# Optimization experiments

Measured on AMD Instinct MI355X. Metric: run time of the kernel, lower is better.

The kernel has to match this reference:

```python
import jax, jax.numpy as jnp
import numpy as np

EMBED_DIM = 768
NUM_HEADS = 12
HEAD_DIM = EMBED_DIM // NUM_HEADS
SCALE = HEAD_DIM ** -0.5


def setup_inputs() -> dict:
    key = jax.random.key(0)
    k_x, k_wqkv, k_bqkv, k_wfc, k_bfc = jax.random.split(key, 5)
    B, S, D = 32, 577, EMBED_DIM
    x = jax.random.normal(k_x, (B, S, D), dtype=jnp.float32)
    # torch Linear default init ~ U(-1/sqrt(fan_in), 1/sqrt(fan_in)); scale suffices
    lim = 1.0 / np.sqrt(D)
    w_qkv = jax.random.uniform(k_wqkv, (D, 3 * D), jnp.float32, -lim, lim)
    b_qkv = jax.random.uniform(k_bqkv, (3 * D,), jnp.float32, -lim, lim)
    w_fc = jax.random.uniform(k_wfc, (D, D), jnp.float32, -lim, lim)
    b_fc = jax.random.uniform(k_bfc, (D,), jnp.float32, -lim, lim)
    return {"x": x, "w_qkv": w_qkv, "b_qkv": b_qkv, "w_fc": w_fc, "b_fc": b_fc}


def reference(x, w_qkv, b_qkv, w_fc, b_fc):
    B, S, D = x.shape
    H, Dh = NUM_HEADS, HEAD_DIM
    qkv = x @ w_qkv + b_qkv                      # [B,S,3D]
    qkv = qkv.reshape(B, S, 3, H, Dh)
    q, k, v = jnp.moveaxis(qkv, 2, 0)            # each [B,S,H,Dh]
    # scores: [B,H,S,S]
    attn = jnp.einsum('bqhd,bkhd->bhqk', q, k) * SCALE
    attn = jax.nn.softmax(attn, axis=-1)
    out = jnp.einsum('bhqk,bkhd->bqhd', attn, v).reshape(B, S, D)
    # dropout in eval mode -> identity
    return out @ w_fc + b_fc
```

## Files before the change

### kernel.cpp

```cpp
#include <hip/hip_runtime.h>
#include <hip/hip_bf16.h>
#include <stdint.h>

typedef __attribute__((ext_vector_type(8))) short short8;
typedef __attribute__((ext_vector_type(4))) float f32x4;

typedef __attribute__((address_space(3))) uint8_t lds_u8;
typedef __attribute__((address_space(1))) uint8_t glb_u8;

__device__ __forceinline__ void load_lds_16(const void* g, void* l) {
    __builtin_amdgcn_global_load_lds((glb_u8*)g, (lds_u8*)l, 16, 0, 0);
}

__device__ __forceinline__ unsigned short f2b(float f) {
    __hip_bfloat16 h = __float2bfloat16(f);
    return __builtin_bit_cast(unsigned short, h);
}
__device__ __forceinline__ ushort2 f2b2(float a, float b) {
    __hip_bfloat162 h = __float22bfloat162_rn(float2{a, b});
    ushort2 r;
    __builtin_memcpy(&r, &h, sizeof(r));
    return r;
}
__device__ __forceinline__ float b2f(unsigned short u) {
    unsigned int x = ((unsigned int)u) << 16;
    return __builtin_bit_cast(float, x);
}

constexpr int Bz = 32, Ss = 577, Dd = 768, Hh = 12;
constexpr int Mm = Bz * Ss;
constexpr int QKV_N = 3 * Dd;
constexpr float SCALE_L2E = 0.125f * 1.4426950408889634f;

__global__ void cast_f32_bf16(const float* __restrict__ src,
                              unsigned short* __restrict__ dst, int n4) {
    int i = blockIdx.x * blockDim.x + threadIdx.x;
    if (i >= n4) return;
    float4 v = ((const float4*)src)[i];
    ushort4 o;
    o.x = f2b(v.x); o.y = f2b(v.y); o.z = f2b(v.z); o.w = f2b(v.w);
    ((ushort4*)dst)[i] = o;
}

__global__ void transpose_cast(const float* __restrict__ src,
                               unsigned short* __restrict__ dst, int R, int C) {
    __shared__ unsigned short tile[32][33];
    int c0 = blockIdx.x * 32, r0 = blockIdx.y * 32;
    int tx = threadIdx.x, ty = threadIdx.y;
#pragma unroll
    for (int i = 0; i < 4; ++i)
        tile[ty + i * 8][tx] = f2b(src[(size_t)(r0 + ty + i * 8) * C + c0 + tx]);
    __syncthreads();
#pragma unroll
    for (int i = 0; i < 4; ++i) {
        int rr = ty + i * 8;
        dst[(size_t)(c0 + rr) * R + r0 + tx] = tile[tx][rr];
    }
}

template <int N_, bool OUT_BF16>
__global__ __launch_bounds__(512, 2)
void gemm256(const unsigned short* __restrict__ A,
             const unsigned short* __restrict__ Bt,
             const float* __restrict__ bias,
             void* __restrict__ Cout) {
    constexpr int K = 768;
    constexpr int KB = 12;
    constexpr int NX = N_ / 256;
    constexpr int NY = (Mm + 255) / 256;
    constexpr int NWG = NX * NY;
    constexpr int QC = NWG >> 3, RC = NWG & 7;
    extern __shared__ __align__(16) uint8_t smem[];

    const int tid = threadIdx.x;
    const int wave = tid >> 6, lane = tid & 63;
    const int quad = lane >> 4, lc = lane & 15;
    const int wm = wave >> 2, wn = wave & 3;

    const int orig = blockIdx.y * NX + blockIdx.x;
    const int xcd = orig & 7, lid = orig >> 3;
    const int wgid = (xcd < RC ? xcd * (QC + 1) : RC * (QC + 1) + (xcd - RC) * QC) + lid;
    const int tm = (wgid / NX) * 256;
    const int tn = (wgid % NX) * 256;

    const int colsw = ((lane & 7) ^ (lane >> 3)) * 8;
    const unsigned short* rpA[2][2];
    const unsigned short* rpB[2][2];
#pragma unroll
    for (int s = 0; s < 2; ++s) {
        const int prs = (s * 8 + wave) * 8 + (lane >> 3);
#pragma unroll
        for (int h = 0; h < 2; ++h) {
            int ar = tm + (prs >> 6) * 128 + h * 64 + (prs & 63);
            if (ar >= Mm) ar = Mm - 1;
            rpA[s][h] = A + (size_t)ar * K + colsw;
            int br = tn + (prs >> 5) * 64 + h * 32 + (prs & 31);
            rpB[s][h] = Bt + (size_t)br * K + colsw;
        }
    }

    auto ldsA = [&](int b, int mh) -> uint8_t* { return smem + b * 65536 + mh * 16384; };
    auto ldsB = [&](int b, int nh) -> uint8_t* { return smem + b * 65536 + 32768 + nh * 16384; };

    auto stageA = [&](int kb, int mh) {
        uint8_t* d = ldsA(kb & 1, mh) + wave * 1024;
        load_lds_16(rpA[0][mh] + kb * 64, d);
        load_lds_16(rpA[1][mh] + kb * 64, d + 8192);
    };
    auto stageB = [&](int kb, int nh) {
        uint8_t* d = ldsB(kb & 1, nh) + wave * 1024;
        load_lds_16(rpB[0][nh] + kb * 64, d);
        load_lds_16(rpB[1][nh] + kb * 64, d + 8192);
    };

    short8 af[2][4], bf[2][2];
    auto readA = [&](int b, int mh) {
        const unsigned short* p = (const unsigned short*)ldsA(b, mh);
#pragma unroll
        for (int i = 0; i < 4; ++i) {
            const int pr = wm * 64 + i * 16 + lc;
            const unsigned short* r = p + pr * 64;
            const int sw = pr & 7;
            af[0][i] = *(const short8*)(r + ((quad) ^ sw) * 8);
            af[1][i] = *(const short8*)(r + ((4 + quad) ^ sw) * 8);
        }
    };
    auto readB = [&](int b, int nh) {
        const unsigned short* p = (const unsigned short*)ldsB(b, nh);
#pragma unroll
        for (int j = 0; j < 2; ++j) {
            const int pr = wn * 32 + j * 16 + lc;
            const unsigned short* r = p + pr * 64;
            const int sw = pr & 7;
            bf[0][j] = *(const short8*)(r + ((quad) ^ sw) * 8);
            bf[1][j] = *(const short8*)(r + ((4 + quad) ^ sw) * 8);
        }
    };

    f32x4 acc[8][4] = {};
    auto quadmfma = [&](int mh, int nh) {
        __builtin_amdgcn_s_setprio(1);
#pragma unroll
        for (int ks = 0; ks < 2; ++ks)
#pragma unroll
            for (int i = 0; i < 4; ++i)
#pragma unroll
                for (int j = 0; j < 2; ++j)
                    acc[mh * 4 + i][nh * 2 + j] = __builtin_amdgcn_mfma_f32_16x16x32_bf16(
                        af[ks][i], bf[ks][j], acc[mh * 4 + i][nh * 2 + j], 0, 0, 0);
        __builtin_amdgcn_s_setprio(0);
    };

    stageA(0, 0); stageB(0, 1); stageA(0, 1); stageB(0, 0);
    stageA(1, 0); stageB(1, 1);
    asm volatile("s_waitcnt vmcnt(4)" ::: "memory");
    __builtin_amdgcn_s_barrier();

    for (int T = 0; T < KB; ++T) {
        const int rb = T & 1;
        readA(rb, 0); readB(rb, 0);
        if (T + 1 < KB) stageA(T + 1, 1);
        __builtin_amdgcn_s_barrier();
        asm volatile("s_waitcnt lgkmcnt(0)" ::: "memory");
        quadmfma(0, 0);
        __builtin_amdgcn_s_barrier();
        readB(rb, 1);
        if (T + 1 < KB) stageB(T + 1, 0);
        __builtin_amdgcn_s_barrier();
        asm volatile("s_waitcnt lgkmcnt(0)" ::: "memory");
        quadmfma(0, 1);
        __builtin_amdgcn_s_barrier();
        readA(rb, 1);
        if (T + 2 < KB) stageA(T + 2, 0);
        __builtin_amdgcn_s_barrier();
        asm volatile("s_waitcnt lgkmcnt(0)" ::: "memory");
        quadmfma(1, 1);
        __builtin_amdgcn_s_barrier();
        readB(rb, 0);
        if (T + 2 < KB) stageB(T + 2, 1);
        __builtin_amdgcn_s_barrier();
        asm volatile("s_waitcnt lgkmcnt(0)" ::: "memory");
        quadmfma(1, 0);
        if (T + 2 < KB) { asm volatile("s_waitcnt vmcnt(4)" ::: "memory"); }
        else            { asm volatile("s_waitcnt vmcnt(0)" ::: "memory"); }
        __builtin_amdgcn_s_barrier();
    }

    float bv[4];
#pragma unroll
    for (int j = 0; j < 4; ++j) bv[j] = bias[tn + wn * 64 + j * 16 + lc];

    float* ep = (float*)smem + wave * (16 * 68);
    const int erow = lane >> 2, ec = (lane & 3) * 16;
#pragma unroll
    for (int ia = 0; ia < 8; ++ia) {
#pragma unroll
        for (int j = 0; j < 4; ++j)
#pragma unroll
            for (int r = 0; r < 4; ++r)
                ep[(quad * 4 + r) * 68 + j * 16 + lc] = acc[ia][j][r] + bv[j];
        __threadfence_block();
        int grow = tm + wm * 128 + ia * 16 + erow;
        if (grow < Mm) {
            float4 c0 = *(float4*)&ep[erow * 68 + ec + 0];
            float4 c1 = *(float4*)&ep[erow * 68 + ec + 4];
            float4 c2 = *(float4*)&ep[erow * 68 + ec + 8];
            float4 c3 = *(float4*)&ep[erow * 68 + ec + 12];
            int gcol = tn + wn * 64 + ec;
            if constexpr (OUT_BF16) {
                unsigned short o[16];
                *(ushort2*)&o[0]  = f2b2(c0.x, c0.y);
                *(ushort2*)&o[2]  = f2b2(c0.z, c0.w);
                *(ushort2*)&o[4]  = f2b2(c1.x, c1.y);
                *(ushort2*)&o[6]  = f2b2(c1.z, c1.w);
                *(ushort2*)&o[8]  = f2b2(c2.x, c2.y);
                *(ushort2*)&o[10] = f2b2(c2.z, c2.w);
                *(ushort2*)&o[12] = f2b2(c3.x, c3.y);
                *(ushort2*)&o[14] = f2b2(c3.z, c3.w);
                unsigned short* op = (unsigned short*)Cout + (size_t)grow * N_ + gcol;
                *(short8*)(op + 0) = *(short8*)&o[0];
                *(short8*)(op + 8) = *(short8*)&o[8];
            } else {
                float* op = (float*)Cout + (size_t)grow * N_ + gcol;
                *(float4*)(op + 0)  = c0;
                *(float4*)(op + 4)  = c1;
                *(float4*)(op + 8)  = c2;
                *(float4*)(op + 12) = c3;
            }
        }
        __threadfence_block();
    }
}

__device__ __forceinline__ void attn_tile(
    const unsigned short* __restrict__ Ktile,
    const unsigned short* __restrict__ Vtb,
    unsigned short* __restrict__ Pqw,
    const short8& qf0, const short8& qf1,
    int quad, int lc,
    f32x4 (&oacc)[4], f32x4& lacc) {

    const int sw = lc & 7;
    f32x4 sfr[4];
    __builtin_amdgcn_s_setprio(1);
#pragma unroll
    for (int f = 0; f < 4; ++f) {
        const unsigned short* kr = Ktile + (f * 16 + lc) * 64;
        short8 k0 = *(const short8*)(kr + (quad ^ sw) * 8);
        short8 k1 = *(const short8*)(kr + ((quad ^ 4) ^ sw) * 8);
        f32x4 z = {};
        z = __builtin_amdgcn_mfma_f32_16x16x32_bf16(k0, qf0, z, 0, 0, 0);
        z = __builtin_amdgcn_mfma_f32_16x16x32_bf16(k1, qf1, z, 0, 0, 0);
        sfr[f] = z;
    }
    __builtin_amdgcn_s_setprio(0);

#pragma unroll
    for (int f = 0; f < 4; ++f) {
        float p[4];
#pragma unroll
        for (int r = 0; r < 4; ++r)
            p[r] = __builtin_amdgcn_exp2f(sfr[f][r] * SCALE_L2E);
        ushort2 lo = f2b2(p[0], p[1]), hi = f2b2(p[2], p[3]);
        ushort4 pk = {lo.x, lo.y, hi.x, hi.y};
        *(ushort4*)&Pqw[lc * 72 + f * 16 + quad * 4] = pk;
    }

    __threadfence_block();

    short8 pf0 = *(const short8*)&Pqw[lc * 72 + quad * 8];
    short8 pf1 = *(const short8*)&Pqw[lc * 72 + 32 + quad * 8];
    __builtin_amdgcn_s_setprio(1);
#pragma unroll
    for (int g = 0; g < 4; ++g) {
        short8 vf0 = *(const short8*)&Vtb[(g * 16 + lc) * 80 + quad * 8];
        short8 vf1 = *(const short8*)&Vtb[(g * 16 + lc) * 80 + 32 + quad * 8];
        oacc[g] = __builtin_amdgcn_mfma_f32_16x16x32_bf16(vf0, pf0, oacc[g], 0, 0, 0);
        oacc[g] = __builtin_amdgcn_mfma_f32_16x16x32_bf16(vf1, pf1, oacc[g], 0, 0, 0);
    }
    short8 vo0 = *(const short8*)&Vtb[(64 + lc) * 80 + quad * 8];
    short8 vo1 = *(const short8*)&Vtb[(64 + lc) * 80 + 32 + quad * 8];
    lacc = __builtin_amdgcn_mfma_f32_16x16x32_bf16(vo0, pf0, lacc, 0, 0, 0);
    lacc = __builtin_amdgcn_mfma_f32_16x16x32_bf16(vo1, pf1, lacc, 0, 0, 0);
    __builtin_amdgcn_s_setprio(0);
}

__global__ __launch_bounds__(512)
void attn_kernel(const unsigned short* __restrict__ qkv,
                 unsigned short* __restrict__ outb) {
    __shared__ unsigned short Kt[2][64 * 64];
    __shared__ unsigned short Vt[2][80 * 80];
    __shared__ unsigned short Pq[8][16 * 72];

    const int tid = threadIdx.x;
    const int wave = tid >> 6, lane = tid & 63;
    const int quad = lane >> 4, lc = lane & 15;

    const int orig = (blockIdx.z * gridDim.y + blockIdx.y) * gridDim.x + blockIdx.x;
    const int wgid = (orig & 7) * 240 + (orig >> 3);
    const int qt = wgid % 5;
    const int h  = (wgid / 5) % Hh;
    const int b  = wgid / (5 * Hh);

    const unsigned short* qkvK = qkv + (size_t)b * Ss * QKV_N + h * 64 + 768;
    const unsigned short* qkvV = qkvK + 768;

    const int krow = lane >> 3;
    const int gch = (lane & 7) ^ krow;

    const int qbase = qt * 128 + wave * 16;
    int qrow = qbase + lc; if (qrow > Ss - 1) qrow = Ss - 1;
    const unsigned short* qp = qkv + (size_t)(b * Ss + qrow) * QKV_N + h * 64;
    short8 qf0 = *(const short8*)(qp + quad * 8);
    short8 qf1 = *(const short8*)(qp + 32 + quad * 8);

    unsigned short* Pqw = Pq[wave];

    auto stage_K = [&](int tile, int buf) {
        int key = tile * 64 + wave * 8 + krow;
        const unsigned short* gp = qkvK + (size_t)key * QKV_N + gch * 8;
        load_lds_16(gp, (void*)&Kt[buf][wave * 512]);
    };
    auto load_V = [&](int tile) -> short8 {
        int key = tile * 64 + lane;
        return *(const short8*)(qkvV + (size_t)key * QKV_N + wave * 8);
    };
    auto write_V = [&](short8 v, int buf) {
#pragma unroll
        for (int j = 0; j < 8; ++j)
            Vt[buf][(wave * 8 + j) * 80 + lane] = (unsigned short)v[j];
    };

    if (tid < 80) {
        Vt[0][64 * 80 + tid] = 0x3F80;
        Vt[1][64 * 80 + tid] = 0x3F80;
    }

    f32x4 oacc[4] = {};
    f32x4 lacc = {};

    stage_K(0, 0);
    write_V(load_V(0), 0);
    __syncthreads();

    for (int kb = 0; kb < 8; ++kb) {
        const int buf = kb & 1;
        stage_K(kb + 1, buf ^ 1);
        short8 vreg = load_V(kb + 1);
        attn_tile(Kt[buf], Vt[buf], Pqw, qf0, qf1, quad, lc, oacc, lacc);
        write_V(vreg, buf ^ 1);
        __syncthreads();
    }
    attn_tile(Kt[0], Vt[0], Pqw, qf0, qf1, quad, lc, oacc, lacc);

    float ptail;
    {
        const unsigned short* k576 = qkvK + (size_t)576 * QKV_N;
        short8 kk0 = *(const short8*)(k576 + quad * 8);
        short8 kk1 = *(const short8*)(k576 + 32 + quad * 8);
        float part = 0.f;
#pragma unroll
        for (int j = 0; j < 8; ++j)
            part += b2f((unsigned short)qf0[j]) * b2f((unsigned short)kk0[j])
                  + b2f((unsigned short)qf1[j]) * b2f((unsigned short)kk1[j]);
        part += __shfl_xor(part, 16, 64);
        part += __shfl_xor(part, 32, 64);
        ptail = __builtin_amdgcn_exp2f(part * SCALE_L2E);
        const unsigned short* v576 = qkvV + (size_t)576 * QKV_N;
#pragma unroll
        for (int g = 0; g < 4; ++g) {
            ushort4 vv = *(const ushort4*)(v576 + g * 16 + quad * 4);
            oacc[g][0] += ptail * b2f(vv.x);
            oacc[g][1] += ptail * b2f(vv.y);
            oacc[g][2] += ptail * b2f(vv.z);
            oacc[g][3] += ptail * b2f(vv.w);
        }
    }

    float lq = __shfl(lacc[0], lc, 64) + ptail;
    float inv = 1.f / lq;
#pragma unroll
    for (int g = 0; g < 4; ++g) {
        ushort2 lo = f2b2(oacc[g][0] * inv, oacc[g][1] * inv);
        ushort2 hi = f2b2(oacc[g][2] * inv, oacc[g][3] * inv);
        ushort4 ob = {lo.x, lo.y, hi.x, hi.y};
        *(ushort4*)&Pqw[lc * 72 + g * 16 + quad * 4] = ob;
    }
    __threadfence_block();
#pragma unroll
    for (int p = 0; p < 2; ++p) {
        int lr = p * 8 + (lane >> 3), ch = lane & 7;
        int q = qbase + lr;
        if (q <= Ss - 1) {
            short8 vv = *(const short8*)&Pqw[lr * 72 + ch * 8];
            *(short8*)(outb + (size_t)(b * Ss + q) * Dd + h * 64 + ch * 8) = vv;
        }
    }
}

extern "C" void kernel_launch(void* const* d_in, const int* in_sizes, int n_in,
                              void* d_out, int out_size, void* d_ws, size_t ws_size,
                              hipStream_t stream) {
    const float* x     = (const float*)d_in[0];
    const float* w_qkv = (const float*)d_in[1];
    const float* b_qkv = (const float*)d_in[2];
    const float* w_fc  = (const float*)d_in[3];
    const float* b_fc  = (const float*)d_in[4];

    uint8_t* ws = (uint8_t*)d_ws;
    unsigned short* xb    = (unsigned short*)(ws + 0);
    unsigned short* wqkvT = (unsigned short*)(ws + 28360704);
    unsigned short* wfcT  = (unsigned short*)(ws + 31899648);
    unsigned short* qkv   = (unsigned short*)(ws + 33079296);
    unsigned short* attn  = (unsigned short*)(ws + 118161408);

    static bool lds_init = false;
    if (!lds_init) {
        hipFuncSetAttribute((const void*)gemm256<QKV_N, true>,
                            hipFuncAttributeMaxDynamicSharedMemorySize, 131072);
        hipFuncSetAttribute((const void*)gemm256<Dd, false>,
                            hipFuncAttributeMaxDynamicSharedMemorySize, 131072);
        lds_init = true;
    }

    int n4 = (Mm * Dd) / 4;
    cast_f32_bf16<<<(n4 + 255) / 256, 256, 0, stream>>>(x, xb, n4);
    transpose_cast<<<dim3(QKV_N / 32, Dd / 32), dim3(32, 8), 0, stream>>>(w_qkv, wqkvT, Dd, QKV_N);
    transpose_cast<<<dim3(Dd / 32, Dd / 32), dim3(32, 8), 0, stream>>>(w_fc, wfcT, Dd, Dd);

    gemm256<QKV_N, true><<<dim3(QKV_N / 256, (Mm + 255) / 256), 512, 131072, stream>>>(xb, wqkvT, b_qkv, qkv);

    attn_kernel<<<dim3(5, Hh, Bz), 512, 0, stream>>>(qkv, attn);

    gemm256<Dd, false><<<dim3(Dd / 256, (Mm + 255) / 256), 512, 131072, stream>>>(attn, wfcT, b_fc, d_out);
}
```

Measured before the change: 308.1 us.

## Simplify GEMM main loop to one-tile-ahead double buffering with single barrier

Replaces the fine-grained four-phase schedule with a plain double-buffered loop. The old loop staged half-tiles two iterations ahead and put barriers around each MFMA quarter. The new loop issues all global-to-LDS loads for the next K tile up front, runs the four MFMA quarters back to back, then waits for all outstanding loads and syncs once per iteration. This cuts barrier and wait overhead. In exchange it shortens prefetch depth to one tile and waits on every outstanding global load each iteration, which may expose memory latency. Sched barriers are added to stop the compiler moving work across the loop boundary.

```diff
diff --git a/kernel.cpp b/kernel.cpp
--- a/kernel.cpp
+++ b/kernel.cpp
@@ -151,39 +151,29 @@
         __builtin_amdgcn_s_setprio(0);
     };
 
-    stageA(0, 0); stageB(0, 1); stageA(0, 1); stageB(0, 0);
-    stageA(1, 0); stageB(1, 1);
-    asm volatile("s_waitcnt vmcnt(4)" ::: "memory");
+    stageA(0, 0); stageA(0, 1); stageB(0, 0); stageB(0, 1);
+    asm volatile("s_waitcnt vmcnt(0)" ::: "memory");
     __builtin_amdgcn_s_barrier();
+    __builtin_amdgcn_sched_barrier(0);
 
     for (int T = 0; T < KB; ++T) {
         const int rb = T & 1;
-        readA(rb, 0); readB(rb, 0);
-        if (T + 1 < KB) stageA(T + 1, 1);
+        readA(rb, 0);
+        readB(rb, 0);
+        if (T + 1 < KB) {
+            stageA(T + 1, 0); stageA(T + 1, 1);
+            stageB(T + 1, 0); stageB(T + 1, 1);
+        }
+        quadmfma(0, 0);
+        readB(rb, 1);
+        quadmfma(0, 1);
+        readA(rb, 1);
+        quadmfma(1, 1);
+        readB(rb, 0);
+        quadmfma(1, 0);
+        asm volatile("s_waitcnt vmcnt(0)" ::: "memory");
         __builtin_amdgcn_s_barrier();
-        asm volatile("s_waitcnt lgkmcnt(0)" ::: "memory");
-        quadmfma(0, 0);
-        __builtin_amdgcn_s_barrier();
-        readB(rb, 1);
-        if (T + 1 < KB) stageB(T + 1, 0);
-        __builtin_amdgcn_s_barrier();
-        asm volatile("s_waitcnt lgkmcnt(0)" ::: "memory");
-        quadmfma(0, 1);
-        __builtin_amdgcn_s_barrier();
-        readA(rb, 1);
-        if (T + 2 < KB) stageA(T + 2, 0);
-        __builtin_amdgcn_s_barrier();
-        asm volatile("s_waitcnt lgkmcnt(0)" ::: "memory");
-        quadmfma(1, 1);
-        __builtin_amdgcn_s_barrier();
-        readB(rb, 0);
-        if (T + 2 < KB) stageB(T + 2, 1);
-        __builtin_amdgcn_s_barrier();
-        asm volatile("s_waitcnt lgkmcnt(0)" ::: "memory");
-        quadmfma(1, 0);
-        if (T + 2 < KB) { asm volatile("s_waitcnt vmcnt(4)" ::: "memory"); }
-        else            { asm volatile("s_waitcnt vmcnt(0)" ::: "memory"); }
-        __builtin_amdgcn_s_barrier();
+        __builtin_amdgcn_sched_barrier(0);
     }
 
     float bv[4];
```

Result: no change. 308.0 us (-0.0%).
